# Kernel optimization log

Measured on AMD Instinct MI355X. Metric: run time of the kernel, lower is better.

## Reference

```python
import jax, jax.numpy as jnp
import numpy as np

REG_COEF = 0.001


def setup_inputs() -> dict:
    key = jax.random.key(0)
    k1, k2, k3, k4 = jax.random.split(key, 4)
    B, K, d = 8192, 1024, 64
    q = jax.random.normal(k1, (B, d), dtype=jnp.float32)
    c = jax.random.normal(k2, (K, d), dtype=jnp.float32)
    # positive bandwidths, as produced by adjust_bandwidth (1/(2*rho^2))
    bandwidth = jax.random.uniform(k3, (K,), dtype=jnp.float32, minval=0.1, maxval=1.0)
    g_inv_c = jax.random.normal(k4, (K, d, d), dtype=jnp.float32)
    return {"q": q, "c": c, "bandwidth": bandwidth, "g_inv_c": g_inv_c}


def reference(q, c, bandwidth, g_inv_c):
    # squared euclidean distances: ||q-c||^2, computed via the expanded form
    sq_q = jnp.sum(q * q, axis=-1, keepdims=True)           # (B,1)
    sq_c = jnp.sum(c * c, axis=-1)                          # (K,)
    d2 = jnp.maximum(sq_q + sq_c[None, :] - 2.0 * (q @ c.T), 0.0)  # (B,K)
    weights = jnp.exp(-bandwidth[None, :] * d2)             # (B,K)
    g_inv = jnp.einsum('bk,kij->bij', weights, g_inv_c)     # (B,d,d)
    d = q.shape[-1]
    g_inv = g_inv + REG_COEF * jnp.eye(d, dtype=q.dtype)[None, :, :]
    return g_inv
```

## Files before the change

kernel.cpp:

```cpp
#include <hip/hip_runtime.h>
#include <hip/hip_bf16.h>

typedef __attribute__((ext_vector_type(8))) short bf16x8;
typedef __attribute__((ext_vector_type(4))) float f32x4;

#define Bsz 8192
#define Ksz 1024
#define Dsz 64
#define Nsz 4096

__device__ __forceinline__ void async_load16(const void* g, void* lds) {
    __builtin_amdgcn_global_load_lds(
        (const __attribute__((address_space(1))) void*)g,
        (__attribute__((address_space(3))) void*)lds,
        16, 0, 0);
}

__device__ __forceinline__ float bf2f(unsigned short s) {
    union { unsigned u; float f; } x;
    x.u = ((unsigned)s) << 16;
    return x.f;
}

__global__ __launch_bounds__(256) void transpose_convert(
    const float* __restrict__ G, __hip_bfloat16* __restrict__ Gt)
{
    __shared__ float tile[64][65];
    const int t = threadIdx.x;
    const int n0 = blockIdx.x * 64;
    const int k0 = blockIdx.y * 64;

    for (int i = 0; i < 4; ++i) {
        int f4 = t + 256 * i;
        int row = f4 >> 4;
        int c4  = (f4 & 15) << 2;
        float4 v = *(const float4*)&G[(size_t)(k0 + row) * Nsz + n0 + c4];
        tile[row][c4 + 0] = v.x;
        tile[row][c4 + 1] = v.y;
        tile[row][c4 + 2] = v.z;
        tile[row][c4 + 3] = v.w;
    }
    __syncthreads();
    for (int i = 0; i < 4; ++i) {
        int o = t + 256 * i;
        int rowp = o >> 4;
        int c4   = (o & 15) << 2;
        union { ushort4 u; __hip_bfloat16 h[4]; } cvt;
        cvt.h[0] = __float2bfloat16(tile[c4 + 0][rowp]);
        cvt.h[1] = __float2bfloat16(tile[c4 + 1][rowp]);
        cvt.h[2] = __float2bfloat16(tile[c4 + 2][rowp]);
        cvt.h[3] = __float2bfloat16(tile[c4 + 3][rowp]);
        *(ushort4*)&Gt[(size_t)(n0 + rowp) * Ksz + k0 + c4] = cvt.u;
    }
}

#define QSTR 72

__global__ __launch_bounds__(256) void weights_mfma(
    const float* __restrict__ q, const float* __restrict__ c,
    const float* __restrict__ bw, __hip_bfloat16* __restrict__ W)
{
    __shared__ __attribute__((aligned(16))) __hip_bfloat16 qh[128 * QSTR];
    __shared__ __attribute__((aligned(16))) __hip_bfloat16 ql[128 * QSTR];
    __shared__ __attribute__((aligned(16))) __hip_bfloat16 ch[128 * QSTR];
    __shared__ __attribute__((aligned(16))) __hip_bfloat16 cl[128 * QSTR];
    __shared__ float sqq[128];
    __shared__ float sqc[128];

    const int t  = threadIdx.x;
    const int b0 = blockIdx.x * 128;
    const int k0 = blockIdx.y * 128;

    for (int i = 0; i < 8; ++i) {
        int f4  = t + 256 * i;
        int row = f4 >> 4;
        int c4  = (f4 & 15) << 2;
        float4 v = *(const float4*)&q[(size_t)(b0 + row) * Dsz + c4];
        float4 u = *(const float4*)&c[(size_t)(k0 + row) * Dsz + c4];
        float qv[4] = {v.x, v.y, v.z, v.w};
        float cv[4] = {2.f * u.x, 2.f * u.y, 2.f * u.z, 2.f * u.w};
        union { ushort4 u4; __hip_bfloat16 h[4]; } qhh, qll, chh, cll;
        #pragma unroll
        for (int e = 0; e < 4; ++e) {
            __hip_bfloat16 hb = __float2bfloat16(qv[e]);
            qhh.h[e] = hb;
            qll.h[e] = __float2bfloat16(qv[e] - bf2f(*(unsigned short*)&hb));
            __hip_bfloat16 hc = __float2bfloat16(cv[e]);
            chh.h[e] = hc;
            cll.h[e] = __float2bfloat16(cv[e] - bf2f(*(unsigned short*)&hc));
        }
        *(ushort4*)&qh[row * QSTR + c4] = qhh.u4;
        *(ushort4*)&ql[row * QSTR + c4] = qll.u4;
        *(ushort4*)&ch[row * QSTR + c4] = chh.u4;
        *(ushort4*)&cl[row * QSTR + c4] = cll.u4;
    }
    __syncthreads();

    if (t < 128) {
        float s = 0.f;
        for (int x8 = 0; x8 < 64; x8 += 8) {
            bf16x8 h = *(const bf16x8*)&qh[t * QSTR + x8];
            bf16x8 l = *(const bf16x8*)&ql[t * QSTR + x8];
            #pragma unroll
            for (int e = 0; e < 8; ++e) {
                float v = bf2f((unsigned short)h[e]) + bf2f((unsigned short)l[e]);
                s += v * v;
            }
        }
        sqq[t] = s;
    } else {
        int r = t - 128;
        float s = 0.f;
        for (int x8 = 0; x8 < 64; x8 += 8) {
            bf16x8 h = *(const bf16x8*)&ch[r * QSTR + x8];
            bf16x8 l = *(const bf16x8*)&cl[r * QSTR + x8];
            #pragma unroll
            for (int e = 0; e < 8; ++e) {
                float v = 0.5f * (bf2f((unsigned short)h[e]) + bf2f((unsigned short)l[e]));
                s += v * v;
            }
        }
        sqc[r] = s;
    }
    __syncthreads();

    const int wave = t >> 6;
    const int lane = t & 63;
    const int wm = (wave >> 1) * 64;
    const int wn = (wave & 1) * 64;
    const int lrow = lane & 15;
    const int lk8  = (lane >> 4) << 3;

    f32x4 acc[4][4];
    for (int i = 0; i < 4; ++i)
        for (int j = 0; j < 4; ++j) acc[i][j] = (f32x4){0.f, 0.f, 0.f, 0.f};

    #pragma unroll
    for (int ks = 0; ks < 64; ks += 32) {
        bf16x8 ah[4], al[4], bh[4], bl[4];
        #pragma unroll
        for (int i = 0; i < 4; ++i) {
            int ra = (wm + i * 16 + lrow) * QSTR + ks + lk8;
            int rb = (wn + i * 16 + lrow) * QSTR + ks + lk8;
            ah[i] = *(const bf16x8*)&qh[ra];
            al[i] = *(const bf16x8*)&ql[ra];
            bh[i] = *(const bf16x8*)&ch[rb];
            bl[i] = *(const bf16x8*)&cl[rb];
        }
        #pragma unroll
        for (int i = 0; i < 4; ++i)
            #pragma unroll
            for (int j = 0; j < 4; ++j) {
                acc[i][j] = __builtin_amdgcn_mfma_f32_16x16x32_bf16(ah[i], bh[j], acc[i][j], 0, 0, 0);
                acc[i][j] = __builtin_amdgcn_mfma_f32_16x16x32_bf16(ah[i], bl[j], acc[i][j], 0, 0, 0);
                acc[i][j] = __builtin_amdgcn_mfma_f32_16x16x32_bf16(al[i], bh[j], acc[i][j], 0, 0, 0);
            }
    }

    const int crow = (lane >> 4) << 2;
    const int ccol = lane & 15;
    for (int j = 0; j < 4; ++j) {
        int k = wn + j * 16 + ccol;
        float bwv = bw[k0 + k];
        float sc  = sqc[k];
        #pragma unroll
        for (int i = 0; i < 4; ++i) {
            #pragma unroll
            for (int r = 0; r < 4; ++r) {
                int b = wm + i * 16 + crow + r;
                float d2 = fmaxf(sqq[b] + sc - acc[i][j][r], 0.f);
                W[(size_t)(b0 + b) * Ksz + (k0 + k)] = __float2bfloat16(__expf(-bwv * d2));
            }
        }
    }
}

#define TM2 256
#define TN2 256
#define BK2 64
#define NT  (Ksz / BK2)

#define BAR()        __builtin_amdgcn_s_barrier()
#define WAIT_LGKM0() asm volatile("s_waitcnt lgkmcnt(0)" ::: "memory")

#define MFMA_QUAD(B, MO, NO)                                                   \
    _Pragma("unroll")                                                          \
    for (int ks = 0; ks < 2; ++ks)                                             \
        _Pragma("unroll")                                                      \
        for (int m = 0; m < 4; ++m)                                            \
            _Pragma("unroll")                                                  \
            for (int n = 0; n < 2; ++n)                                        \
                acc[MO + m][NO + n] = __builtin_amdgcn_mfma_f32_16x16x32_bf16( \
                    a[ks][m], B[ks][n], acc[MO + m][NO + n], 0, 0, 0);

__global__ __launch_bounds__(512, 2) void gemm_8ph(
    const __hip_bfloat16* __restrict__ A,
    const __hip_bfloat16* __restrict__ Bt,
    float* __restrict__ C)
{
    __shared__ __attribute__((aligned(16))) __hip_bfloat16 As[2 * 2 * 128 * 64];
    __shared__ __attribute__((aligned(16))) __hip_bfloat16 Bs[2 * 2 * 128 * 64];

    const int t    = threadIdx.x;
    const int wave = t >> 6;
    const int lane = t & 63;

    const int wg  = blockIdx.x;
    const int swz = (wg & 7) * (512 / 8) + (wg >> 3);
    const int bx  = swz & 15;
    const int by  = swz >> 4;
    const int m0  = by * TM2;
    const int n0  = bx * TN2;

    const int wm   = (wave >> 2) * 128;
    const int wn   = (wave & 3) * 64;
    const int lrow = lane & 15;
    const int kg   = lane >> 4;

    f32x4 acc[8][4];
    #pragma unroll
    for (int i = 0; i < 8; ++i)
        #pragma unroll
        for (int j = 0; j < 4; ++j) acc[i][j] = (f32x4){0.f, 0.f, 0.f, 0.f};

    auto stageA = [&](int tt, int h) {
        __hip_bfloat16* lds = &As[(((tt & 1) << 1) + h) * 8192];
        const int row0 = m0 + (h << 6);
        const int kcol = tt << 6;
        #pragma unroll
        for (int l = 0; l < 2; ++l) {
            int ch   = (l << 9) + t;
            int rl   = ch >> 3;
            int g8   = (ch & 7) ^ (rl & 7);
            int grow = row0 + ((rl >> 6) << 7) + (rl & 63);
            async_load16(A + (size_t)grow * Ksz + kcol + (g8 << 3), lds + (ch << 3));
        }
    };
    auto stageB = [&](int tt, int h) {
        __hip_bfloat16* lds = &Bs[(((tt & 1) << 1) + h) * 8192];
        const int row0 = n0 + (h << 5);
        const int kcol = tt << 6;
        #pragma unroll
        for (int l = 0; l < 2; ++l) {
            int ch   = (l << 9) + t;
            int rl   = ch >> 3;
            int g8   = (ch & 7) ^ (rl & 7);
            int grow = row0 + ((rl >> 5) << 6) + (rl & 31);
            async_load16(Bt + (size_t)grow * Ksz + kcol + (g8 << 3), lds + (ch << 3));
        }
    };

    bf16x8 a[2][4], b0[2][2], b1[2][2];

    auto readA = [&](int bb, int mh) {
        const __hip_bfloat16* base = &As[((bb << 1) + mh) * 8192];
        #pragma unroll
        for (int ks = 0; ks < 2; ++ks)
            #pragma unroll
            for (int m = 0; m < 4; ++m) {
                int rl = (wm >> 1) + m * 16 + lrow;
                int cc = ((((ks << 2) + kg) ^ (rl & 7)) << 3);
                a[ks][m] = *(const bf16x8*)&base[rl * 64 + cc];
            }
    };
    auto readB = [&](bf16x8 (&b)[2][2], int bb, int nh) {
        const __hip_bfloat16* base = &Bs[((bb << 1) + nh) * 8192];
        #pragma unroll
        for (int ks = 0; ks < 2; ++ks)
            #pragma unroll
            for (int n = 0; n < 2; ++n) {
                int rl = (wn >> 1) + n * 16 + lrow;
                int cc = ((((ks << 2) + kg) ^ (rl & 7)) << 3);
                b[ks][n] = *(const bf16x8*)&base[rl * 64 + cc];
            }
    };

    stageA(0, 0); stageA(0, 1); stageB(0, 0); stageB(0, 1);
    stageA(1, 0); stageB(1, 0); stageB(1, 1);
    asm volatile("s_waitcnt vmcnt(6)" ::: "memory");
    BAR();

    #pragma unroll 2
    for (int tt = 0; tt < NT; ++tt) {
        const int buf = tt & 1;

        readA(buf, 0);
        readB(b0, buf, 0);
        if (tt + 1 < NT) stageA(tt + 1, 1);
        asm volatile("s_waitcnt lgkmcnt(8)" ::: "memory");
        BAR();
        WAIT_LGKM0();
        __builtin_amdgcn_s_setprio(1);
        MFMA_QUAD(b0, 0, 0);
        __builtin_amdgcn_s_setprio(0);
        BAR();

        readB(b1, buf, 1);
        if (tt + 2 < NT) stageA(tt + 2, 0);
        BAR();
        WAIT_LGKM0();
        __builtin_amdgcn_s_setprio(1);
        MFMA_QUAD(b1, 0, 2);
        __builtin_amdgcn_s_setprio(0);
        BAR();

        readA(buf, 1);
        if (tt + 2 < NT) stageB(tt + 2, 0);
        BAR();
        WAIT_LGKM0();
        __builtin_amdgcn_s_setprio(1);
        MFMA_QUAD(b1, 4, 2);
        __builtin_amdgcn_s_setprio(0);
        BAR();

        if (tt + 2 < NT) stageB(tt + 2, 1);
        BAR();
        WAIT_LGKM0();
        __builtin_amdgcn_s_setprio(1);
        MFMA_QUAD(b0, 4, 0);
        __builtin_amdgcn_s_setprio(0);
        if (tt < NT - 2) {
            asm volatile("s_waitcnt vmcnt(6)" ::: "memory");
        } else if (tt == NT - 2) {
            asm volatile("s_waitcnt vmcnt(0)" ::: "memory");
        }
        BAR();
    }

    const int crow = (lane >> 4) << 2;
    const int ccol = lane & 15;
    #pragma unroll
    for (int nj = 0; nj < 4; ++nj) {
        int gn = n0 + wn + ((nj >> 1) << 5) + ((nj & 1) << 4) + ccol;
        float diag = (gn % 65 == 0) ? 0.001f : 0.f;
        #pragma unroll
        for (int mi = 0; mi < 8; ++mi) {
            int gmb = m0 + wm + ((mi >> 2) << 6) + ((mi & 3) << 4) + crow;
            #pragma unroll
            for (int r = 0; r < 4; ++r) {
                __builtin_nontemporal_store(acc[mi][nj][r] + diag,
                                            &C[(size_t)(gmb + r) * Nsz + gn]);
            }
        }
    }
}

extern "C" void kernel_launch(void* const* d_in, const int* in_sizes, int n_in,
                              void* d_out, int out_size, void* d_ws, size_t ws_size,
                              hipStream_t stream) {
    const float* q  = (const float*)d_in[0];
    const float* c  = (const float*)d_in[1];
    const float* bw = (const float*)d_in[2];
    const float* G  = (const float*)d_in[3];
    float* out = (float*)d_out;

    __hip_bfloat16* W  = (__hip_bfloat16*)d_ws;
    __hip_bfloat16* Gt = (__hip_bfloat16*)((char*)d_ws + (size_t)16 * 1024 * 1024);

    transpose_convert<<<dim3(Nsz / 64, Ksz / 64), 256, 0, stream>>>(G, Gt);
    weights_mfma<<<dim3(Bsz / 128, Ksz / 128), 256, 0, stream>>>(q, c, bw, W);
    gemm_8ph<<<dim3((Bsz / TM2) * (Nsz / TN2)), 512, 0, stream>>>(W, Gt, out);
}
```

Measured before the change: 229.1 us.

## Make GEMM blocks process two M tiles with a continuous cross-tile prefetch pipeline

Each GEMM workgroup now computes two consecutive 256-row output tiles, halving the grid from 512 to 256 blocks. The K-loop is extended to 32 steps so the prefetch of the second tile's first K slices overlaps the tail of the first tile, and the accumulators are written out and reset mid-loop. This removes per-block prologue and epilogue pipeline bubbles, but it leaves fewer blocks than two per CU on a 256-CU part and keeps the first tile's C stores inside the loop.

Result: slower. 295.6 us (+29.0%).

```diff
diff --git a/kernel.cpp b/kernel.cpp
--- a/kernel.cpp
+++ b/kernel.cpp
@@ -178,7 +178,7 @@
 #define TM2 256
 #define TN2 256
 #define BK2 64
-#define NT  (Ksz / BK2)
+#define NTT 32
 
 #define BAR()        __builtin_amdgcn_s_barrier()
 #define WAIT_LGKM0() asm volatile("s_waitcnt lgkmcnt(0)" ::: "memory")
@@ -206,10 +206,10 @@
     const int lane = t & 63;
 
     const int wg  = blockIdx.x;
-    const int swz = (wg & 7) * (512 / 8) + (wg >> 3);
+    const int swz = (wg & 7) * 32 + (wg >> 3);
     const int bx  = swz & 15;
-    const int by  = swz >> 4;
-    const int m0  = by * TM2;
+    const int byq = swz >> 4;
+    const int m0  = byq * 512;
     const int n0  = bx * TN2;
 
     const int wm   = (wave >> 2) * 128;
@@ -223,10 +223,10 @@
         #pragma unroll
         for (int j = 0; j < 4; ++j) acc[i][j] = (f32x4){0.f, 0.f, 0.f, 0.f};
 
-    auto stageA = [&](int tt, int h) {
-        __hip_bfloat16* lds = &As[(((tt & 1) << 1) + h) * 8192];
-        const int row0 = m0 + (h << 6);
-        const int kcol = tt << 6;
+    auto stageA = [&](int gtt, int h) {
+        __hip_bfloat16* lds = &As[(((gtt & 1) << 1) + h) * 8192];
+        const int row0 = m0 + ((gtt >> 4) << 8) + (h << 6);
+        const int kcol = (gtt & 15) << 6;
         #pragma unroll
         for (int l = 0; l < 2; ++l) {
             int ch   = (l << 9) + t;
@@ -236,10 +236,10 @@
             async_load16(A + (size_t)grow * Ksz + kcol + (g8 << 3), lds + (ch << 3));
         }
     };
-    auto stageB = [&](int tt, int h) {
-        __hip_bfloat16* lds = &Bs[(((tt & 1) << 1) + h) * 8192];
+    auto stageB = [&](int gtt, int h) {
+        __hip_bfloat16* lds = &Bs[(((gtt & 1) << 1) + h) * 8192];
         const int row0 = n0 + (h << 5);
-        const int kcol = tt << 6;
+        const int kcol = (gtt & 15) << 6;
         #pragma unroll
         for (int l = 0; l < 2; ++l) {
             int ch   = (l << 9) + t;
@@ -275,18 +275,37 @@
             }
     };
 
+    const int crow = (lane >> 4) << 2;
+    const int ccol = lane & 15;
+    auto dumpC = [&](int mbase) {
+        #pragma unroll
+        for (int nj = 0; nj < 4; ++nj) {
+            int gn = n0 + wn + ((nj >> 1) << 5) + ((nj & 1) << 4) + ccol;
+            float diag = (gn % 65 == 0) ? 0.001f : 0.f;
+            #pragma unroll
+            for (int mi = 0; mi < 8; ++mi) {
+                int gmb = mbase + wm + ((mi >> 2) << 6) + ((mi & 3) << 4) + crow;
+                #pragma unroll
+                for (int r = 0; r < 4; ++r) {
+                    __builtin_nontemporal_store(acc[mi][nj][r] + diag,
+                                                &C[(size_t)(gmb + r) * Nsz + gn]);
+                }
+            }
+        }
+    };
+
     stageA(0, 0); stageA(0, 1); stageB(0, 0); stageB(0, 1);
     stageA(1, 0); stageB(1, 0); stageB(1, 1);
     asm volatile("s_waitcnt vmcnt(6)" ::: "memory");
     BAR();
 
     #pragma unroll 2
-    for (int tt = 0; tt < NT; ++tt) {
-        const int buf = tt & 1;
+    for (int gtt = 0; gtt < NTT; ++gtt) {
+        const int buf = gtt & 1;
 
         readA(buf, 0);
         readB(b0, buf, 0);
-        if (tt + 1 < NT) stageA(tt + 1, 1);
+        if (gtt + 1 < NTT) stageA(gtt + 1, 1);
         asm volatile("s_waitcnt lgkmcnt(8)" ::: "memory");
         BAR();
         WAIT_LGKM0();
@@ -296,7 +315,7 @@
         BAR();
 
         readB(b1, buf, 1);
-        if (tt + 2 < NT) stageA(tt + 2, 0);
+        if (gtt + 2 < NTT) stageA(gtt + 2, 0);
         BAR();
         WAIT_LGKM0();
         __builtin_amdgcn_s_setprio(1);
@@ -305,7 +324,7 @@
         BAR();
 
         readA(buf, 1);
-        if (tt + 2 < NT) stageB(tt + 2, 0);
+        if (gtt + 2 < NTT) stageB(gtt + 2, 0);
         BAR();
         WAIT_LGKM0();
         __builtin_amdgcn_s_setprio(1);
@@ -313,36 +332,29 @@
         __builtin_amdgcn_s_setprio(0);
         BAR();
 
-        if (tt + 2 < NT) stageB(tt + 2, 1);
+        if (gtt + 2 < NTT) stageB(gtt + 2, 1);
         BAR();
         WAIT_LGKM0();
         __builtin_amdgcn_s_setprio(1);
         MFMA_QUAD(b0, 4, 0);
         __builtin_amdgcn_s_setprio(0);
-        if (tt < NT - 2) {
+        if (gtt < NTT - 2) {
             asm volatile("s_waitcnt vmcnt(6)" ::: "memory");
-        } else if (tt == NT - 2) {
+        } else if (gtt == NTT - 2) {
             asm volatile("s_waitcnt vmcnt(0)" ::: "memory");
         }
         BAR();
-    }
-
-    const int crow = (lane >> 4) << 2;
-    const int ccol = lane & 15;
-    #pragma unroll
-    for (int nj = 0; nj < 4; ++nj) {
-        int gn = n0 + wn + ((nj >> 1) << 5) + ((nj & 1) << 4) + ccol;
-        float diag = (gn % 65 == 0) ? 0.001f : 0.f;
-        #pragma unroll
-        for (int mi = 0; mi < 8; ++mi) {
-            int gmb = m0 + wm + ((mi >> 2) << 6) + ((mi & 3) << 4) + crow;
-            #pragma unroll
-            for (int r = 0; r < 4; ++r) {
-                __builtin_nontemporal_store(acc[mi][nj][r] + diag,
-                                            &C[(size_t)(gmb + r) * Nsz + gn]);
-            }
-        }
-    }
+
+        if (gtt == 15) {
+            dumpC(m0);
+            #pragma unroll
+            for (int i = 0; i < 8; ++i)
+                #pragma unroll
+                for (int j = 0; j < 4; ++j) acc[i][j] = (f32x4){0.f, 0.f, 0.f, 0.f};
+        }
+    }
+
+    dumpC(m0 + 256);
 }
 
 extern "C" void kernel_launch(void* const* d_in, const int* in_sizes, int n_in,
@@ -359,5 +371,5 @@
 
     transpose_convert<<<dim3(Nsz / 64, Ksz / 64), 256, 0, stream>>>(G, Gt);
     weights_mfma<<<dim3(Bsz / 128, Ksz / 128), 256, 0, stream>>>(q, c, bw, W);
-    gemm_8ph<<<dim3((Bsz / TM2) * (Nsz / TN2)), 512, 0, stream>>>(W, Gt, out);
-}
+    gemm_8ph<<<dim3(256), 512, 0, stream>>>(W, Gt, out);
+}
```

## Double-buffer A fragments and prefetch next tile's LDS reads during MFMA

Applied to the files above, without the earlier changes.

Restructures the 8-phase GEMM main loop so each tile's first A and B fragments are read from LDS at the end of the previous iteration, and A fragments use two register sets (aC, aN). The fixed lgkmcnt(0) waits become partial lgkmcnt/vmcnt counts so LDS reads overlap with MFMA work. Tail guards are dropped by wrapping the k column with (tt & 15), which issues redundant loads past the end and keeps the waits uniform. This uses more registers, which could hurt occupancy at the 2-blocks launch bound, and the hand-tuned wait counts risk race conditions.

Measured after the change: 222.7 us. -2.8%, faster.

```diff
diff --git a/kernel.cpp b/kernel.cpp
--- a/kernel.cpp
+++ b/kernel.cpp
@@ -178,12 +178,11 @@
 #define TM2 256
 #define TN2 256
 #define BK2 64
-#define NT  (Ksz / BK2)
-
-#define BAR()        __builtin_amdgcn_s_barrier()
-#define WAIT_LGKM0() asm volatile("s_waitcnt lgkmcnt(0)" ::: "memory")
-
-#define MFMA_QUAD(B, MO, NO)                                                   \
+#define NT2 16
+
+#define BAR()  __builtin_amdgcn_s_barrier()
+
+#define MFMA_QUAD(Aa, Bb, MO, NO)                                              \
     _Pragma("unroll")                                                          \
     for (int ks = 0; ks < 2; ++ks)                                             \
         _Pragma("unroll")                                                      \
@@ -191,7 +190,7 @@
             _Pragma("unroll")                                                  \
             for (int n = 0; n < 2; ++n)                                        \
                 acc[MO + m][NO + n] = __builtin_amdgcn_mfma_f32_16x16x32_bf16( \
-                    a[ks][m], B[ks][n], acc[MO + m][NO + n], 0, 0, 0);
+                    Aa[ks][m], Bb[ks][n], acc[MO + m][NO + n], 0, 0, 0);
 
 __global__ __launch_bounds__(512, 2) void gemm_8ph(
     const __hip_bfloat16* __restrict__ A,
@@ -206,7 +205,7 @@
     const int lane = t & 63;
 
     const int wg  = blockIdx.x;
-    const int swz = (wg & 7) * (512 / 8) + (wg >> 3);
+    const int swz = (wg & 7) * 64 + (wg >> 3);
     const int bx  = swz & 15;
     const int by  = swz >> 4;
     const int m0  = by * TM2;
@@ -226,7 +225,7 @@
     auto stageA = [&](int tt, int h) {
         __hip_bfloat16* lds = &As[(((tt & 1) << 1) + h) * 8192];
         const int row0 = m0 + (h << 6);
-        const int kcol = tt << 6;
+        const int kcol = (tt & 15) << 6;
         #pragma unroll
         for (int l = 0; l < 2; ++l) {
             int ch   = (l << 9) + t;
@@ -239,7 +238,7 @@
     auto stageB = [&](int tt, int h) {
         __hip_bfloat16* lds = &Bs[(((tt & 1) << 1) + h) * 8192];
         const int row0 = n0 + (h << 5);
-        const int kcol = tt << 6;
+        const int kcol = (tt & 15) << 6;
         #pragma unroll
         for (int l = 0; l < 2; ++l) {
             int ch   = (l << 9) + t;
@@ -250,9 +249,9 @@
         }
     };
 
-    bf16x8 a[2][4], b0[2][2], b1[2][2];
-
-    auto readA = [&](int bb, int mh) {
+    bf16x8 aC[2][4], aN[2][4], b0[2][2], b1[2][2];
+
+    auto readA = [&](bf16x8 (&a)[2][4], int bb, int mh) {
         const __hip_bfloat16* base = &As[((bb << 1) + mh) * 8192];
         #pragma unroll
         for (int ks = 0; ks < 2; ++ks)
@@ -275,55 +274,53 @@
             }
     };
 
-    stageA(0, 0); stageA(0, 1); stageB(0, 0); stageB(0, 1);
-    stageA(1, 0); stageB(1, 0); stageB(1, 1);
-    asm volatile("s_waitcnt vmcnt(6)" ::: "memory");
+    stageA(0, 0); stageB(0, 0);
+    stageB(0, 1); stageA(0, 1); stageA(1, 0); stageB(1, 0); stageB(1, 1);
+    asm volatile("s_waitcnt vmcnt(10)" ::: "memory");
     BAR();
+    readA(aC, 0, 0);
+    readB(b0, 0, 0);
 
     #pragma unroll 2
-    for (int tt = 0; tt < NT; ++tt) {
+    for (int tt = 0; tt < NT2; ++tt) {
         const int buf = tt & 1;
 
-        readA(buf, 0);
-        readB(b0, buf, 0);
-        if (tt + 1 < NT) stageA(tt + 1, 1);
+        asm volatile("s_waitcnt vmcnt(8)" ::: "memory");
+        BAR();
+        readB(b1, buf, 1);
+        stageA(tt + 1, 1);
+        asm volatile("s_waitcnt lgkmcnt(4)" ::: "memory");
+        __builtin_amdgcn_s_setprio(1);
+        MFMA_QUAD(aC, b0, 0, 0);
+        __builtin_amdgcn_s_setprio(0);
+        BAR();
+
+        asm volatile("s_waitcnt vmcnt(8)" ::: "memory");
+        BAR();
+        readA(aN, buf, 1);
+        stageA(tt + 2, 0);
         asm volatile("s_waitcnt lgkmcnt(8)" ::: "memory");
-        BAR();
-        WAIT_LGKM0();
         __builtin_amdgcn_s_setprio(1);
-        MFMA_QUAD(b0, 0, 0);
+        MFMA_QUAD(aC, b1, 0, 2);
         __builtin_amdgcn_s_setprio(0);
         BAR();
 
-        readB(b1, buf, 1);
-        if (tt + 2 < NT) stageA(tt + 2, 0);
-        BAR();
-        WAIT_LGKM0();
+        stageB(tt + 2, 0);
+        BAR();
+        asm volatile("s_waitcnt lgkmcnt(0)" ::: "memory");
         __builtin_amdgcn_s_setprio(1);
-        MFMA_QUAD(b1, 0, 2);
+        MFMA_QUAD(aN, b1, 4, 2);
         __builtin_amdgcn_s_setprio(0);
         BAR();
 
-        readA(buf, 1);
-        if (tt + 2 < NT) stageB(tt + 2, 0);
-        BAR();
-        WAIT_LGKM0();
+        stageB(tt + 2, 1);
+        asm volatile("s_waitcnt vmcnt(10)" ::: "memory");
+        BAR();
         __builtin_amdgcn_s_setprio(1);
-        MFMA_QUAD(b1, 4, 2);
+        MFMA_QUAD(aN, b0, 4, 0);
         __builtin_amdgcn_s_setprio(0);
-        BAR();
-
-        if (tt + 2 < NT) stageB(tt + 2, 1);
-        BAR();
-        WAIT_LGKM0();
-        __builtin_amdgcn_s_setprio(1);
-        MFMA_QUAD(b0, 4, 0);
-        __builtin_amdgcn_s_setprio(0);
-        if (tt < NT - 2) {
-            asm volatile("s_waitcnt vmcnt(6)" ::: "memory");
-        } else if (tt == NT - 2) {
-            asm volatile("s_waitcnt vmcnt(0)" ::: "memory");
-        }
+        readA(aC, buf ^ 1, 0);
+        readB(b0, buf ^ 1, 0);
         BAR();
     }
 
```
